# Performance work log

Measured on AMD Instinct MI355X. Metric: run time of the kernel, lower is better.

The kernel has to match this reference:

```python
import jax, jax.numpy as jnp
import numpy as np

P = 22536   # priors
B = 32      # batch
M = 16      # objects per image (fixed for jit)
C = 81      # classes incl. background
THRESHOLD = 0.5
ALPHA_REG = 1.0   # config.reg_weights
FL_ALPHA = 0.25
FL_GAMMA = 2.0
EPS = 1e-7


def cxcy_to_xy(c):
    return jnp.concatenate([c[..., :2] - c[..., 2:] / 2, c[..., :2] + c[..., 2:] / 2], -1)


def gcxgcy_to_cxcy(g, p):
    return jnp.concatenate([g[..., :2] * p[..., 2:] / 10 + p[..., :2],
                            jnp.exp(g[..., 2:] / 5) * p[..., 2:]], -1)


def iou_xy(a, b):
    # a: (M,4) xyxy, b: (P,4) xyxy -> (M,P)
    lt = jnp.maximum(a[:, None, :2], b[None, :, :2])
    rb = jnp.minimum(a[:, None, 2:], b[None, :, 2:])
    inter = jnp.prod(jnp.clip(rb - lt, 0.0), -1)
    area_a = jnp.prod(a[:, 2:] - a[:, :2], -1)
    area_b = jnp.prod(b[:, 2:] - b[:, :2], -1)
    return inter / (area_a[:, None] + area_b[None, :] - inter)


def diou_loss(p, g):
    # elementwise DIoU loss, p/g: (..., 4) xyxy -> (...)
    lt = jnp.maximum(p[..., :2], g[..., :2])
    rb = jnp.minimum(p[..., 2:], g[..., 2:])
    inter = jnp.prod(jnp.clip(rb - lt, 0.0), -1)
    ap = jnp.prod(p[..., 2:] - p[..., :2], -1)
    ag = jnp.prod(g[..., 2:] - g[..., :2], -1)
    iou = inter / (ap + ag - inter + EPS)
    cp = (p[..., :2] + p[..., 2:]) / 2
    cg = (g[..., :2] + g[..., 2:]) / 2
    d2 = jnp.sum((cp - cg) ** 2, -1)
    elt = jnp.minimum(p[..., :2], g[..., :2])
    erb = jnp.maximum(p[..., 2:], g[..., 2:])
    c2 = jnp.sum((erb - elt) ** 2, -1) + EPS
    return 1.0 - iou + d2 / c2


def match_image(boxes_i, labels_i, priors_xy):
    # boxes_i: (M,4), labels_i: (M,), priors_xy: (P,4)
    overlap = iou_xy(boxes_i, priors_xy)                 # (M,P)
    ofp = overlap.max(0)                                  # overlap_for_each_prior (P,)
    obj = jnp.argmax(overlap, 0)                          # object_for_each_prior (P,)
    pfo = jnp.argmax(overlap, 1)                          # prior_for_each_object (M,)
    obj = obj.at[pfo].set(jnp.arange(M))
    ofp = ofp.at[pfo].set(1.0)
    lab = labels_i[obj]                                   # (P,)
    lab_neg = jnp.where(ofp < THRESHOLD - 0.1, -1, lab)
    lab = jnp.where(ofp < THRESHOLD, 0, lab)
    true_locs = boxes_i[obj]                              # (P,4)
    return lab, lab_neg, true_locs


def setup_inputs() -> dict:
    key = jax.random.key(0)
    k1, k2, k3, k4, k5, k6, k7 = jax.random.split(key, 7)
    pcxy = jax.random.uniform(k1, (P, 2), minval=0.05, maxval=0.95)
    pwh = jax.random.uniform(k2, (P, 2), minval=0.02, maxval=0.3)
    priors_cxcy = jnp.concatenate([pcxy, pwh], -1)
    ctr = jax.random.uniform(k3, (B, M, 2), minval=0.2, maxval=0.8)
    wh = jax.random.uniform(k4, (B, M, 2), minval=0.05, maxval=0.3)
    boxes = jnp.concatenate([ctr - wh / 2, ctr + wh / 2], -1)
    labels = jax.random.randint(k5, (B, M), 1, C).astype(jnp.int32)
    predicted_locs = jax.random.normal(k6, (B, P, 4), dtype=jnp.float32)
    predicted_scores = jax.random.normal(k7, (B, P, C), dtype=jnp.float32)
    return {"predicted_locs": predicted_locs, "predicted_scores": predicted_scores,
            "boxes": boxes, "labels": labels, "priors_cxcy": priors_cxcy}


def reference(predicted_locs, predicted_scores, boxes, labels, priors_cxcy):
    priors_xy = cxcy_to_xy(priors_cxcy)
    lab, lab_neg, true_locs = jax.vmap(match_image, in_axes=(0, 0, None))(boxes, labels, priors_xy)
    decoded = cxcy_to_xy(gcxgcy_to_cxcy(predicted_locs, priors_cxcy))   # (B,P,4)
    pos = lab > 0
    neg = lab_neg == -1
    # DIoU localization loss, mean over positive priors
    loc = diou_loss(decoded, true_locs)                                 # (B,P)
    npos = jnp.maximum(pos.sum(), 1)
    loc_loss = jnp.sum(loc * pos) / npos
    # focal classification loss over union of positive and hard-negative priors
    logp = jax.nn.log_softmax(predicted_scores, -1)                     # (B,P,C)
    lp_t = jnp.take_along_axis(logp, lab[..., None], -1)[..., 0]        # (B,P)
    pt = jnp.exp(lp_t)
    fl = FL_ALPHA * (1.0 - pt) ** FL_GAMMA * (-lp_t)
    m = pos | neg
    conf_loss = jnp.sum(fl * m) / jnp.maximum(m.sum(), 1)
    return conf_loss + ALPHA_REG * loc_loss
```

## Files before the change

### kernel.cpp

```cpp
#include <hip/hip_runtime.h>
#include <math.h>

#define PN 22536
#define BN 32
#define MN 16
#define CN 81
#define NMB ((PN + 255) / 256)

#if __has_builtin(__builtin_amdgcn_exp2f)
#define EXP2(x) __builtin_amdgcn_exp2f(x)
#else
#define EXP2(x) exp2f(x)
#endif
#if __has_builtin(__builtin_amdgcn_logf)
#define LOG2(x) __builtin_amdgcn_logf(x)
#else
#define LOG2(x) log2f(x)
#endif

__global__ __launch_bounds__(256)
void pfo_kernel(const float* __restrict__ boxes,
                const float* __restrict__ priors,
                unsigned long long* __restrict__ pfo_key)
{
    const int b = blockIdx.y;
    const int p = blockIdx.x * 256 + threadIdx.x;

    __shared__ float4 sbox[MN];
    __shared__ float  sarea[MN];
    __shared__ unsigned long long skey[MN];
    if (threadIdx.x < MN) {
        float4 bx = reinterpret_cast<const float4*>(boxes)[b * MN + threadIdx.x];
        sbox[threadIdx.x]  = bx;
        sarea[threadIdx.x] = (bx.z - bx.x) * (bx.w - bx.y);
        skey[threadIdx.x]  = 0ull;
    }
    __syncthreads();

    float x0 = 0.f, y0 = 0.f, x1 = 0.f, y1 = 0.f, ab = 0.f;
    const bool valid = (p < PN);
    if (valid) {
        float4 pc = reinterpret_cast<const float4*>(priors)[p];
        float hw = pc.z / 2.0f, hh = pc.w / 2.0f;
        x0 = pc.x - hw; y0 = pc.y - hh;
        x1 = pc.x + hw; y1 = pc.y + hh;
        ab = (x1 - x0) * (y1 - y0);
    }

    const int lane = threadIdx.x & 63;
    #pragma unroll
    for (int m = 0; m < MN; ++m) {
        float iou = -INFINITY;
        if (valid) {
            float4 bx = sbox[m];
            float lx = fmaxf(bx.x, x0), ly = fmaxf(bx.y, y0);
            float rx = fminf(bx.z, x1), ry = fminf(bx.w, y1);
            float inter = fmaxf(rx - lx, 0.0f) * fmaxf(ry - ly, 0.0f);
            iou = inter / (sarea[m] + ab - inter);
        }
        float mx = iou;
        #pragma unroll
        for (int off = 1; off < 64; off <<= 1)
            mx = fmaxf(mx, __shfl_xor(mx, off, 64));
        unsigned long long mask = __ballot(iou == mx);
        int lane0 = (int)__ffsll((unsigned long long)mask) - 1;
        if (valid && lane == lane0) {
            unsigned long long key =
                ((unsigned long long)__float_as_uint(iou) << 32) |
                (unsigned long long)(~(unsigned int)p);
            atomicMax(&skey[m], key);
        }
    }
    __syncthreads();
    if (threadIdx.x < MN)
        atomicMax(&pfo_key[b * MN + threadIdx.x], skey[threadIdx.x]);
}

__global__ __launch_bounds__(256)
void match_conf_kernel(const float* __restrict__ boxes,
                       const int*   __restrict__ labels,
                       const float* __restrict__ priors,
                       const float* __restrict__ plocs,
                       const float* __restrict__ scores,
                       const unsigned long long* __restrict__ pfo_key,
                       float4* __restrict__ mpart)
{
    const int b  = blockIdx.y;
    const int p0 = blockIdx.x * 256;
    const int p  = p0 + threadIdx.x;

    __shared__ float4 sbox[MN];
    __shared__ float  sarea[MN];
    __shared__ int    slab[MN];
    __shared__ int    spfo[MN];
    __shared__ unsigned char slb[256];
    __shared__ float4 spack4[4][162];
    __shared__ float  sred[4][4];

    if (threadIdx.x < MN) {
        float4 bx = reinterpret_cast<const float4*>(boxes)[b * MN + threadIdx.x];
        sbox[threadIdx.x]  = bx;
        sarea[threadIdx.x] = (bx.z - bx.x) * (bx.w - bx.y);
        slab[threadIdx.x]  = labels[b * MN + threadIdx.x];
        spfo[threadIdx.x]  = (int)(~(unsigned int)(pfo_key[b * MN + threadIdx.x] &
                                                   0xFFFFFFFFull));
    }
    __syncthreads();

    float loc = 0.f, mc = 0.f, psc = 0.f;
    unsigned char myl = 255;
    if (p < PN) {
        float4 pc = reinterpret_cast<const float4*>(priors)[p];
        float hw = pc.z / 2.0f, hh = pc.w / 2.0f;
        float qx0 = pc.x - hw, qy0 = pc.y - hh;
        float qx1 = pc.x + hw, qy1 = pc.y + hh;
        float ab  = (qx1 - qx0) * (qy1 - qy0);

        float best = -1.0f;
        int bestm = 0;
        #pragma unroll
        for (int m = 0; m < MN; ++m) {
            float4 bx = sbox[m];
            float lx = fmaxf(bx.x, qx0), ly = fmaxf(bx.y, qy0);
            float rx = fminf(bx.z, qx1), ry = fminf(bx.w, qy1);
            float inter = fmaxf(rx - lx, 0.0f) * fmaxf(ry - ly, 0.0f);
            float iou = inter / (sarea[m] + ab - inter);
            if (iou > best) { best = iou; bestm = m; }
        }
        #pragma unroll
        for (int m = 0; m < MN; ++m)
            if (spfo[m] == p) { bestm = m; best = 1.0f; }

        bool pos = best >= 0.5f;
        bool neg = best < 0.4f;
        myl = pos ? (unsigned char)slab[bestm]
                  : (neg ? (unsigned char)0 : (unsigned char)255);
        if (pos || neg) mc = 1.0f;

        if (pos) {
            float4 g = reinterpret_cast<const float4*>(plocs)[(size_t)b * PN + p];
            float cx = g.x * pc.z / 10.0f + pc.x;
            float cy = g.y * pc.w / 10.0f + pc.y;
            float ww = expf(g.z / 5.0f) * pc.z;
            float hh2 = expf(g.w / 5.0f) * pc.w;
            float px0 = cx - ww / 2.0f, py0 = cy - hh2 / 2.0f;
            float px1 = cx + ww / 2.0f, py1 = cy + hh2 / 2.0f;

            float4 gb = sbox[bestm];
            float lx = fmaxf(px0, gb.x), ly = fmaxf(py0, gb.y);
            float rx = fminf(px1, gb.z), ry = fminf(py1, gb.w);
            float inter = fmaxf(rx - lx, 0.f) * fmaxf(ry - ly, 0.f);
            float apx = (px1 - px0) * (py1 - py0);
            float agx = (gb.z - gb.x) * (gb.w - gb.y);
            float iou = inter / (apx + agx - inter + 1e-7f);
            float cpx = (px0 + px1) / 2.0f, cpy = (py0 + py1) / 2.0f;
            float cgx = (gb.x + gb.z) / 2.0f, cgy = (gb.y + gb.w) / 2.0f;
            float dx = cpx - cgx, dy = cpy - cgy;
            float d2 = dx * dx + dy * dy;
            float ex0 = fminf(px0, gb.x), ey0 = fminf(py0, gb.y);
            float ex1 = fmaxf(px1, gb.z), ey1 = fmaxf(py1, gb.w);
            float ew = ex1 - ex0, eh = ey1 - ey0;
            float c2 = ew * ew + eh * eh + 1e-7f;
            loc = 1.0f - iou + d2 / c2;
            psc = 1.0f;
        }
    }
    slb[threadIdx.x] = myl;

    #pragma unroll
    for (int off = 32; off >= 1; off >>= 1) {
        loc += __shfl_down(loc, (unsigned)off, 64);
        mc  += __shfl_down(mc,  (unsigned)off, 64);
        psc += __shfl_down(psc, (unsigned)off, 64);
    }
    const int lane = threadIdx.x & 63;
    const int w    = threadIdx.x >> 6;
    if (lane == 0) { sred[w][0] = loc; sred[w][1] = mc; sred[w][2] = psc; }
    __syncthreads();

    const int g8 = lane >> 3;
    const int j  = lane & 7;
    const float LOG2E = 1.4426950408889634f;
    const float LN2   = 0.6931471805599453f;

    float confs = 0.f;
    for (int it = 0; it < 8; ++it) {
        const int prow = w * 64 + it * 8;
        const int gp   = p0 + prow;
        if (gp < PN) {
            const size_t fbase = ((size_t)b * PN + gp) * (size_t)CN;
            const float4* gsrc = reinterpret_cast<const float4*>(scores + fbase);
            float4* dst = spack4[w];
            dst[lane]      = gsrc[lane];
            dst[lane + 64] = gsrc[lane + 64];
            if (lane < 34) dst[lane + 128] = gsrc[lane + 128];
            const float* rowp =
                reinterpret_cast<const float*>(spack4[w]) + g8 * 81;

            float v[10];
            #pragma unroll
            for (int k = 0; k < 10; ++k) v[k] = rowp[j + 8 * k];
            float v80 = (j == 0) ? rowp[80] : -INFINITY;

            float mx = v80;
            #pragma unroll
            for (int k = 0; k < 10; ++k) mx = fmaxf(mx, v[k]);
            #pragma unroll
            for (int off = 1; off < 8; off <<= 1)
                mx = fmaxf(mx, __shfl_xor(mx, off, 64));

            const float mx2 = mx * LOG2E;
            float es = EXP2(fmaf(v80, LOG2E, -mx2));
            #pragma unroll
            for (int k = 0; k < 10; ++k)
                es += EXP2(fmaf(v[k], LOG2E, -mx2));
            #pragma unroll
            for (int off = 1; off < 8; off <<= 1)
                es += __shfl_xor(es, off, 64);

            const int lb  = slb[prow + g8];
            const int lbe = (lb == 255) ? 0 : lb;
            const float st = rowp[lbe];
            float q  = fmaf(st, LOG2E, -mx2) - LOG2(es);
            float pt = EXP2(q);
            float om = 1.0f - pt;
            float fl = 0.25f * om * om * (-(q * LN2));
            if (j == 0 && lb != 255) confs += fl;
        }
    }

    #pragma unroll
    for (int off = 1; off < 64; off <<= 1)
        confs += __shfl_xor(confs, off, 64);
    if (lane == 0) sred[w][3] = confs;
    __syncthreads();

    if (threadIdx.x == 0) {
        float a = 0.f, bsum = 0.f, c = 0.f, cf = 0.f;
        #pragma unroll
        for (int i = 0; i < 4; ++i) {
            a += sred[i][0]; bsum += sred[i][1]; c += sred[i][2]; cf += sred[i][3];
        }
        mpart[b * NMB + blockIdx.x] = make_float4(a, c, bsum, cf);
    }
}

__global__ __launch_bounds__(256)
void reduce_kernel(const float4* __restrict__ mpart,
                   float* __restrict__ out)
{
    const int NM = BN * NMB;
    float loc = 0.f, pcnt = 0.f, mcnt = 0.f, conf = 0.f;
    for (int i = threadIdx.x; i < NM; i += 256) {
        float4 v = mpart[i];
        loc += v.x; pcnt += v.y; mcnt += v.z; conf += v.w;
    }

    #pragma unroll
    for (int off = 1; off < 64; off <<= 1) {
        loc  += __shfl_xor(loc,  off, 64);
        pcnt += __shfl_xor(pcnt, off, 64);
        mcnt += __shfl_xor(mcnt, off, 64);
        conf += __shfl_xor(conf, off, 64);
    }
    __shared__ float s[4][4];
    int lane = threadIdx.x & 63, w = threadIdx.x >> 6;
    if (lane == 0) { s[w][0] = loc; s[w][1] = pcnt; s[w][2] = mcnt; s[w][3] = conf; }
    __syncthreads();
    if (threadIdx.x == 0) {
        float L = 0.f, Pc = 0.f, Mc = 0.f, Cf = 0.f;
        #pragma unroll
        for (int i = 0; i < 4; ++i) {
            L += s[i][0]; Pc += s[i][1]; Mc += s[i][2]; Cf += s[i][3];
        }
        out[0] = Cf / fmaxf(Mc, 1.0f) + L / fmaxf(Pc, 1.0f);
    }
}

extern "C" void kernel_launch(void* const* d_in, const int* in_sizes, int n_in,
                              void* d_out, int out_size, void* d_ws, size_t ws_size,
                              hipStream_t stream)
{
    const float* plocs  = (const float*)d_in[0];
    const float* scores = (const float*)d_in[1];
    const float* boxes  = (const float*)d_in[2];
    const int*   labels = (const int*)d_in[3];
    const float* priors = (const float*)d_in[4];
    float* out = (float*)d_out;

    char* ws = (char*)d_ws;
    unsigned long long* pfo_key = (unsigned long long*)ws;
    float4* mpart = (float4*)(ws + 4096);

    hipMemsetAsync(pfo_key, 0, BN * MN * sizeof(unsigned long long), stream);

    dim3 gA(NMB, BN);
    pfo_kernel<<<gA, 256, 0, stream>>>(boxes, priors, pfo_key);
    match_conf_kernel<<<gA, 256, 0, stream>>>(boxes, labels, priors, plocs,
                                              scores, pfo_key, mpart);
    reduce_kernel<<<1, 256, 0, stream>>>(mpart, out);
}
```

Before: 358.9 us.

## Prefetch score rows two iterations ahead with double-buffered per-wave LDS

Restructures the per-wave softmax/focal loop so the global loads of score rows are issued two iterations ahead into registers and staged into a double-buffered shared-memory tile one iteration ahead. The loop is fully unrolled. This is meant to hide global memory latency behind the log-softmax arithmetic rather than stalling on each row load. The cost is doubled LDS per block, extra live registers that may lower occupancy, and reliance on wave-lockstep ordering for buffer reuse without barriers.

```diff
diff --git a/kernel.cpp b/kernel.cpp
--- a/kernel.cpp
+++ b/kernel.cpp
@@ -94,7 +94,7 @@
     __shared__ int    slab[MN];
     __shared__ int    spfo[MN];
     __shared__ unsigned char slb[256];
-    __shared__ float4 spack4[4][162];
+    __shared__ float4 spack4[4][2][162];
     __shared__ float  sred[4][4];
 
     if (threadIdx.x < MN) {
@@ -180,22 +180,47 @@
 
     const int g8 = lane >> 3;
     const int j  = lane & 7;
+    const bool v34 = (lane < 34);
     const float LOG2E = 1.4426950408889634f;
     const float LN2   = 0.6931471805599453f;
 
     float confs = 0.f;
+    float4 r0 = make_float4(0, 0, 0, 0), r1 = r0, r2 = r0;
+
+    #define PKVALID(it) ((p0 + w * 64 + (it) * 8) < PN)
+    #define PKADDR(it) (reinterpret_cast<const float4*>(                    \
+        scores + ((size_t)b * PN + (p0 + w * 64 + (it) * 8)) * (size_t)CN))
+
+    if (PKVALID(0)) {
+        const float4* gsrc = PKADDR(0);
+        r0 = gsrc[lane]; r1 = gsrc[lane + 64];
+        if (v34) r2 = gsrc[lane + 128];
+        float4* d = spack4[w][0];
+        d[lane] = r0; d[lane + 64] = r1;
+        if (v34) d[lane + 128] = r2;
+    }
+    if (PKVALID(1)) {
+        const float4* gsrc = PKADDR(1);
+        r0 = gsrc[lane]; r1 = gsrc[lane + 64];
+        if (v34) r2 = gsrc[lane + 128];
+    }
+
+    #pragma unroll
     for (int it = 0; it < 8; ++it) {
-        const int prow = w * 64 + it * 8;
-        const int gp   = p0 + prow;
-        if (gp < PN) {
-            const size_t fbase = ((size_t)b * PN + gp) * (size_t)CN;
-            const float4* gsrc = reinterpret_cast<const float4*>(scores + fbase);
-            float4* dst = spack4[w];
-            dst[lane]      = gsrc[lane];
-            dst[lane + 64] = gsrc[lane + 64];
-            if (lane < 34) dst[lane + 128] = gsrc[lane + 128];
+        if (it + 1 < 8 && PKVALID(it + 1)) {
+            float4* d = spack4[w][(it + 1) & 1];
+            d[lane] = r0; d[lane + 64] = r1;
+            if (v34) d[lane + 128] = r2;
+        }
+        if (it + 2 < 8 && PKVALID(it + 2)) {
+            const float4* gsrc = PKADDR(it + 2);
+            r0 = gsrc[lane]; r1 = gsrc[lane + 64];
+            if (v34) r2 = gsrc[lane + 128];
+        }
+        if (PKVALID(it)) {
+            const int prow = w * 64 + it * 8;
             const float* rowp =
-                reinterpret_cast<const float*>(spack4[w]) + g8 * 81;
+                reinterpret_cast<const float*>(spack4[w][it & 1]) + g8 * 81;
 
             float v[10];
             #pragma unroll
@@ -228,6 +253,8 @@
             if (j == 0 && lb != 255) confs += fl;
         }
     }
+    #undef PKVALID
+    #undef PKADDR
 
     #pragma unroll
     for (int off = 1; off < 64; off <<= 1)
```

Measured after the change: 360.0 us. No clear change (+0.3%).
